# Performance work log

Measured on AMD Instinct MI355X. Metric: run time of the kernel, lower is better.

The kernel has to match this reference:

```python
import jax, jax.numpy as jnp
import numpy as np

N = 100000
E = 6400000
H = 64  # hidden_nf


def setup_inputs() -> dict:
    key = jax.random.key(0)
    ks = jax.random.split(key, 12)
    x = jax.random.normal(ks[0], (N, 3), dtype=jnp.float32)
    vel = jax.random.normal(ks[1], (N, 3), dtype=jnp.float32)
    vel_norm = jax.random.uniform(ks[2], (N, 1), dtype=jnp.float32)
    edge_index = jax.random.randint(ks[3], (2, E), 0, N, dtype=jnp.int32)
    # coord_mlp_vel: Linear(1,H) -> LeakyReLU(0.2) -> Linear(H,1)
    W1 = jax.random.normal(ks[4], (H, 1), dtype=jnp.float32) * (1.0 / np.sqrt(1))
    b1 = jnp.zeros((H,), dtype=jnp.float32)
    W2 = jax.random.normal(ks[5], (1, H), dtype=jnp.float32) * (1.0 / np.sqrt(H))
    b2 = jnp.zeros((1,), dtype=jnp.float32)
    # phi: Linear(1,H) -> LeakyReLU(0.2) -> Linear(H,1,bias=False, xavier gain=0.001) -> Tanh
    Wp1 = jax.random.normal(ks[6], (H, 1), dtype=jnp.float32) * (1.0 / np.sqrt(1))
    bp1 = jnp.zeros((H,), dtype=jnp.float32)
    Wp2 = jax.random.normal(ks[7], (1, H), dtype=jnp.float32) * 0.001
    return {"x": x, "vel_norm": vel_norm, "vel": vel, "edge_index": edge_index,
            "W1": W1, "b1": b1, "W2": W2, "b2": b2,
            "Wp1": Wp1, "bp1": bp1, "Wp2": Wp2}


def reference(x, vel_norm, vel, edge_index, W1, b1, W2, b2, Wp1, bp1, Wp2):
    row, col = edge_index[0], edge_index[1]
    # edge_model: gather endpoint positions, radial distance -> tiny MLP -> scaled diff
    x_diff = x[row] - x[col]                                   # [E, 3]
    radial = jnp.sqrt(jnp.sum(x_diff * x_diff, axis=1, keepdims=True))  # [E, 1]
    h = jax.nn.leaky_relu(radial @ Wp1.T + bp1, 0.2)           # [E, H]
    e_out = jnp.tanh(h @ Wp2.T)                                # [E, 1]
    m_ij = x_diff * e_out                                      # [E, 3]
    # node_model: unsorted_segment_mean over row
    agg_sum = jax.ops.segment_sum(m_ij, row, num_segments=x.shape[0])           # [N, 3]
    cnt = jax.ops.segment_sum(jnp.ones((m_ij.shape[0], 1), m_ij.dtype), row,
                              num_segments=x.shape[0])                           # [N, 1]
    x_out = x + agg_sum / jnp.maximum(cnt, 1.0)
    # velocity term: x + vel * coord_mlp_vel(vel_norm)
    hv = jax.nn.leaky_relu(vel_norm @ W1.T + b1, 0.2)          # [N, H]
    scale = hv @ W2.T + b2                                     # [N, 1]
    return x_out + vel * scale
```

## Files before the change

kernel.cpp:

```cpp
#include <hip/hip_runtime.h>
#include <hip/hip_fp16.h>
#include <math.h>

#define LEAKY 0.2f
#define HDIM 64
#define EPB 2048
#define TPB1 256
#define PERT (EPB / TPB1)
#define RANGE 1024
#define RSH 10
#define KMAX 128
#define NSLICE 12
#define FIXS 4194304.0f
#define INVFIXS (1.0f / 4194304.0f)


__device__ __forceinline__ float fast_tanh(float v) {
    float e = __builtin_amdgcn_exp2f(v * 2.88539008178f);
    return 1.0f - 2.0f * __builtin_amdgcn_rcpf(e + 1.0f);
}

__device__ __forceinline__ float edge_eo(float rad, float C, bool slow,
                                         const float* sW1, const float* sb1,
                                         const float* sW2) {
    if (!slow) return fast_tanh(C * rad);
    float a = 0.f;
    #pragma unroll
    for (int k = 0; k < HDIM; k++) {
        float h = fmaf(rad, sW1[k], sb1[k]);
        h = (h > 0.f) ? h : LEAKY * h;
        a = fmaf(sW2[k], h, a);
    }
    return fast_tanh(a);
}

__global__ void repack_kernel(const float* __restrict__ x, float4* __restrict__ x4, int N) {
    int i = blockIdx.x * blockDim.x + threadIdx.x;
    if (i < N) x4[i] = make_float4(x[3*i], x[3*i+1], x[3*i+2], 0.f);
}

__global__ void repack_h_kernel(const float* __restrict__ x, uint2* __restrict__ xh, int N,
                                const float* __restrict__ Wp1, const float* __restrict__ bp1,
                                const float* __restrict__ Wp2, float* __restrict__ consts) {
    int i = blockIdx.x * blockDim.x + threadIdx.x;
    if (i < N) {
        unsigned hx = __half_as_ushort(__float2half(x[3*i]));
        unsigned hy = __half_as_ushort(__float2half(x[3*i+1]));
        unsigned hz = __half_as_ushort(__float2half(x[3*i+2]));
        xh[i] = make_uint2((hy << 16) | hx, hz);
    }
    if (blockIdx.x == 0 && threadIdx.x < 64) {
        int k = threadIdx.x;
        float w1 = Wp1[k];
        float slope = (w1 >= 0.f) ? 1.f : LEAKY;
        float c = Wp2[k] * w1 * slope;
        float bnz = (bp1[k] != 0.f) ? 1.f : 0.f;
        #pragma unroll
        for (int off = 32; off > 0; off >>= 1) {
            c += __shfl_down(c, off, 64);
            bnz += __shfl_down(bnz, off, 64);
        }
        if (k == 0) { consts[0] = c; consts[1] = bnz; }
    }
}

__device__ __forceinline__ unsigned long long pack_rec(float dx, float dy, float dz,
                                                       float eo, unsigned lid) {
    unsigned hx = __half_as_ushort(__float2half(dx * eo));
    unsigned hy = __half_as_ushort(__float2half(dy * eo));
    unsigned hz = __half_as_ushort(__float2half(dz * eo));
    return (unsigned long long)lid
         | ((unsigned long long)hx << 11)
         | ((unsigned long long)hy << 27)
         | ((unsigned long long)hz << 43);
}

__device__ __forceinline__ uint2 make_record(uint2 ga, uint2 gb, int r,
                                             float C, bool slow,
                                             const float* sW1, const float* sb1,
                                             const float* sW2) {
    float ax = __half2float(__ushort_as_half((unsigned short)(ga.x & 0xFFFF)));
    float ay = __half2float(__ushort_as_half((unsigned short)(ga.x >> 16)));
    float az = __half2float(__ushort_as_half((unsigned short)(ga.y & 0xFFFF)));
    float bx = __half2float(__ushort_as_half((unsigned short)(gb.x & 0xFFFF)));
    float by = __half2float(__ushort_as_half((unsigned short)(gb.x >> 16)));
    float bz = __half2float(__ushort_as_half((unsigned short)(gb.y & 0xFFFF)));
    float dx = ax - bx, dy = ay - by, dz = az - bz;
    float rad = sqrtf(dx*dx + dy*dy + dz*dz);
    float eo = edge_eo(rad, C, slow, sW1, sb1, sW2);
    unsigned long long u = pack_rec(dx, dy, dz, eo, (unsigned)r & (RANGE - 1));
    return make_uint2((unsigned)u, (unsigned)(u >> 32));
}

__global__ __launch_bounds__(TPB1) void count2_kernel(const int* __restrict__ ei,
                                                      unsigned* __restrict__ histG,
                                                      int E, int K) {
    __shared__ unsigned hist[4][KMAX];
    int w = threadIdx.x >> 6;
    for (int k = threadIdx.x; k < 4 * KMAX; k += TPB1) ((unsigned*)hist)[k] = 0;
    __syncthreads();
    const size_t base = (size_t)blockIdx.x * EPB;
    if (base + EPB <= (size_t)E) {
        const int4* p = (const int4*)(ei + base);
        #pragma unroll
        for (int i = 0; i < EPB / 4 / TPB1; i++) {
            int4 v = p[threadIdx.x + i * TPB1];
            atomicAdd(&hist[w][((unsigned)v.x) >> RSH], 1u);
            atomicAdd(&hist[w][((unsigned)v.y) >> RSH], 1u);
            atomicAdd(&hist[w][((unsigned)v.z) >> RSH], 1u);
            atomicAdd(&hist[w][((unsigned)v.w) >> RSH], 1u);
        }
    } else {
        for (size_t e = base + threadIdx.x; e < (size_t)E; e += TPB1)
            atomicAdd(&hist[w][((unsigned)ei[e]) >> RSH], 1u);
    }
    __syncthreads();
    for (int k = threadIdx.x; k < K; k += TPB1)
        histG[(size_t)blockIdx.x * K + k] = hist[0][k] + hist[1][k] + hist[2][k] + hist[3][k];
}

__global__ __launch_bounds__(256) void colscan_kernel(unsigned* __restrict__ histG,
                                                      unsigned* __restrict__ totals,
                                                      int nblk, int K) {
    __shared__ unsigned pa[256], pb[256];
    const int b = blockIdx.x;
    const int t = threadIdx.x;
    const int chunk = (nblk + 255) / 256;
    const int r0 = t * chunk;
    unsigned s = 0;
    for (int i = 0; i < chunk; i++) {
        int r = r0 + i;
        if (r < nblk) s += histG[(size_t)r * K + b];
    }
    pa[t] = s;
    __syncthreads();
    unsigned* src = pa; unsigned* dst = pb;
    for (int off = 1; off < 256; off <<= 1) {
        unsigned v = src[t];
        if (t >= off) v += src[t - off];
        dst[t] = v;
        __syncthreads();
        unsigned* tmp = src; src = dst; dst = tmp;
    }
    unsigned excl = (t > 0) ? src[t - 1] : 0u;
    if (t == 255) totals[b] = src[255];
    unsigned run = excl;
    for (int i = 0; i < chunk; i++) {
        int r = r0 + i;
        if (r < nblk) {
            size_t a = (size_t)r * K + b;
            unsigned v = histG[a];
            histG[a] = run;
            run += v;
        }
    }
}

__global__ __launch_bounds__(TPB1) void fused_kernel(
        const uint2* __restrict__ xh,
        const int* __restrict__ ei,
        const float* __restrict__ Wp1, const float* __restrict__ bp1,
        const float* __restrict__ Wp2, const float* __restrict__ consts,
        const unsigned* __restrict__ histG, const unsigned* __restrict__ totals,
        uint2* __restrict__ recs, int E, int K) {
    __shared__ uint2 stage[EPB];
    __shared__ unsigned char bucket_of[EPB];
    __shared__ unsigned hist[KMAX];
    __shared__ unsigned scanv[KMAX + 1];
    __shared__ unsigned gstart[KMAX];
    __shared__ unsigned sbase[KMAX + 1];
    __shared__ float sW1[HDIM], sb1[HDIM], sW2[HDIM];
    const float C = consts[0];
    const bool slow = (consts[1] != 0.f);
    if (slow) {
        for (int k = threadIdx.x; k < HDIM; k += TPB1) {
            sW1[k] = Wp1[k]; sb1[k] = bp1[k]; sW2[k] = Wp2[k];
        }
    }
    for (int k = threadIdx.x; k < K; k += TPB1) hist[k] = 0;
    if (threadIdx.x < (unsigned)K) sbase[threadIdx.x] = totals[threadIdx.x];
    __syncthreads();

    const size_t base = (size_t)blockIdx.x * EPB;
    const unsigned t = threadIdx.x;
    uint2 rc[PERT];
    unsigned bk[PERT];
    if (base + EPB <= (size_t)E && (E & 3) == 0) {
        const int4* pr = (const int4*)(ei + base);
        const int4* pc = (const int4*)(ei + (size_t)E + base);
        int4 rv0 = pr[t];
        int4 rv1 = pr[t + TPB1];
        int4 cv0 = pc[t];
        int4 cv1 = pc[t + TPB1];
        uint2 ga0 = xh[rv0.x], ga1 = xh[rv0.y], ga2 = xh[rv0.z], ga3 = xh[rv0.w];
        uint2 ga4 = xh[rv1.x], ga5 = xh[rv1.y], ga6 = xh[rv1.z], ga7 = xh[rv1.w];
        uint2 gb0 = xh[cv0.x], gb1 = xh[cv0.y], gb2 = xh[cv0.z], gb3 = xh[cv0.w];
        uint2 gb4 = xh[cv1.x], gb5 = xh[cv1.y], gb6 = xh[cv1.z], gb7 = xh[cv1.w];
        rc[0] = make_record(ga0, gb0, rv0.x, C, slow, sW1, sb1, sW2);
        rc[1] = make_record(ga1, gb1, rv0.y, C, slow, sW1, sb1, sW2);
        rc[2] = make_record(ga2, gb2, rv0.z, C, slow, sW1, sb1, sW2);
        rc[3] = make_record(ga3, gb3, rv0.w, C, slow, sW1, sb1, sW2);
        rc[4] = make_record(ga4, gb4, rv1.x, C, slow, sW1, sb1, sW2);
        rc[5] = make_record(ga5, gb5, rv1.y, C, slow, sW1, sb1, sW2);
        rc[6] = make_record(ga6, gb6, rv1.z, C, slow, sW1, sb1, sW2);
        rc[7] = make_record(ga7, gb7, rv1.w, C, slow, sW1, sb1, sW2);
        bk[0] = (unsigned)rv0.x >> RSH; bk[1] = (unsigned)rv0.y >> RSH;
        bk[2] = (unsigned)rv0.z >> RSH; bk[3] = (unsigned)rv0.w >> RSH;
        bk[4] = (unsigned)rv1.x >> RSH; bk[5] = (unsigned)rv1.y >> RSH;
        bk[6] = (unsigned)rv1.z >> RSH; bk[7] = (unsigned)rv1.w >> RSH;
        #pragma unroll
        for (int i = 0; i < PERT; i++) atomicAdd(&hist[bk[i]], 1u);
    } else {
        #pragma unroll
        for (int i = 0; i < PERT; i++) {
            size_t e = base + (size_t)i * TPB1 + t;
            bk[i] = 0xFFFFFFFFu;
            if (e < (size_t)E) {
                int r = ei[e];
                int c = ei[(size_t)E + e];
                uint2 ga = xh[r], gb = xh[c];
                rc[i] = make_record(ga, gb, r, C, slow, sW1, sb1, sW2);
                bk[i] = (unsigned)r >> RSH;
                atomicAdd(&hist[bk[i]], 1u);
            }
        }
    }
    __syncthreads();
    if (t == 0) {
        unsigned a = 0;
        for (int k = 0; k < K; k++) { scanv[k] = a; a += hist[k]; }
        scanv[K] = a;
    } else if (t == 64) {
        unsigned a = 0;
        for (int k = 0; k < K; k++) { unsigned v = sbase[k]; sbase[k] = a; a += v; }
        sbase[K] = a;
    }
    __syncthreads();
    if (t < (unsigned)K)
        gstart[t] = sbase[t] + histG[(size_t)blockIdx.x * K + t];
    for (int k = t; k < K; k += TPB1) hist[k] = scanv[k];
    __syncthreads();
    #pragma unroll
    for (int i = 0; i < PERT; i++) {
        if (bk[i] != 0xFFFFFFFFu) {
            unsigned slot = atomicAdd(&hist[bk[i]], 1u);
            stage[slot] = rc[i];
            bucket_of[slot] = (unsigned char)bk[i];
        }
    }
    __syncthreads();
    unsigned total = scanv[K];
    for (unsigned j = t; j < total; j += TPB1) {
        unsigned b_ = bucket_of[j];
        recs[(size_t)gstart[b_] + (j - scanv[b_])] = stage[j];
    }
}

__global__ __launch_bounds__(TPB1) void count_kernel(const int* __restrict__ ei,
                                                     unsigned* __restrict__ cnts,
                                                     int E, int K) {
    __shared__ unsigned hist[4][KMAX];
    int w = threadIdx.x >> 6;
    for (int k = threadIdx.x; k < 4 * KMAX; k += TPB1) ((unsigned*)hist)[k] = 0;
    __syncthreads();
    int base = blockIdx.x * EPB;
    #pragma unroll
    for (int i = 0; i < PERT; i++) {
        int e = base + i * TPB1 + threadIdx.x;
        if (e < E) atomicAdd(&hist[w][((unsigned)ei[e]) >> RSH], 1u);
    }
    __syncthreads();
    for (int k = threadIdx.x; k < K; k += TPB1) {
        unsigned t = hist[0][k] + hist[1][k] + hist[2][k] + hist[3][k];
        if (t) atomicAdd(&cnts[k], t);
    }
}

__global__ void scan_kernel(const unsigned* __restrict__ cnts,
                            unsigned* __restrict__ base,
                            unsigned* __restrict__ cursor, int K) {
    if (threadIdx.x == 0) {
        unsigned acc = 0;
        for (int k = 0; k < K; k++) { base[k] = acc; cursor[k] = acc; acc += cnts[k]; }
        base[K] = acc;
    }
}

__global__ void precompute_kernel(const float* __restrict__ Wp1,
                                  const float* __restrict__ bp1,
                                  const float* __restrict__ Wp2,
                                  float* __restrict__ consts) {
    int k = threadIdx.x;
    float w1 = Wp1[k];
    float slope = (w1 >= 0.f) ? 1.f : LEAKY;
    float c = Wp2[k] * w1 * slope;
    float bnz = (bp1[k] != 0.f) ? 1.f : 0.f;
    #pragma unroll
    for (int off = 32; off > 0; off >>= 1) {
        c += __shfl_down(c, off, 64);
        bnz += __shfl_down(bnz, off, 64);
    }
    if (k == 0) { consts[0] = c; consts[1] = bnz; }
}

__global__ __launch_bounds__(TPB1) void bin_kernel(
        const float* __restrict__ x, const float4* __restrict__ x4, int use4,
        const int* __restrict__ ei,
        const float* __restrict__ Wp1, const float* __restrict__ bp1,
        const float* __restrict__ Wp2, const float* __restrict__ consts,
        unsigned* __restrict__ cursor, uint2* __restrict__ recs, int E, int K) {
    __shared__ uint2 stage[EPB];
    __shared__ unsigned char bucket_of[EPB];
    __shared__ unsigned hist[KMAX];
    __shared__ unsigned scanv[KMAX + 1];
    __shared__ unsigned gstart[KMAX];
    __shared__ float sW1[HDIM], sb1[HDIM], sW2[HDIM];
    const float C = consts[0];
    const bool slow = (consts[1] != 0.f);
    if (slow) {
        for (int k = threadIdx.x; k < HDIM; k += TPB1) {
            sW1[k] = Wp1[k]; sb1[k] = bp1[k]; sW2[k] = Wp2[k];
        }
    }
    for (int k = threadIdx.x; k < K; k += TPB1) hist[k] = 0;
    __syncthreads();

    int base = blockIdx.x * EPB;
    uint2 rc[PERT];
    unsigned bk[PERT];
    #pragma unroll
    for (int i = 0; i < PERT; i++) {
        int e = base + i * TPB1 + threadIdx.x;
        bk[i] = 0xFFFFFFFFu;
        if (e < E) {
            int r = ei[e];
            int c = ei[(size_t)E + e];
            float dx, dy, dz;
            if (use4) {
                float4 a = x4[r], b = x4[c];
                dx = a.x - b.x; dy = a.y - b.y; dz = a.z - b.z;
            } else {
                dx = x[3*r]   - x[3*c];
                dy = x[3*r+1] - x[3*c+1];
                dz = x[3*r+2] - x[3*c+2];
            }
            float rad = sqrtf(dx*dx + dy*dy + dz*dz);
            float eo = edge_eo(rad, C, slow, sW1, sb1, sW2);
            unsigned long long u = pack_rec(dx, dy, dz, eo, (unsigned)r & (RANGE - 1));
            rc[i] = make_uint2((unsigned)u, (unsigned)(u >> 32));
            bk[i] = (unsigned)r >> RSH;
            atomicAdd(&hist[bk[i]], 1u);
        }
    }
    __syncthreads();
    if (threadIdx.x == 0) {
        unsigned a = 0;
        for (int k = 0; k < K; k++) { scanv[k] = a; a += hist[k]; }
        scanv[K] = a;
    }
    __syncthreads();
    if (threadIdx.x < (unsigned)K) {
        unsigned c_ = scanv[threadIdx.x + 1] - scanv[threadIdx.x];
        gstart[threadIdx.x] = c_ ? atomicAdd(&cursor[threadIdx.x], c_) : 0u;
    }
    for (int k = threadIdx.x; k < K; k += TPB1) hist[k] = scanv[k];
    __syncthreads();
    #pragma unroll
    for (int i = 0; i < PERT; i++) {
        if (bk[i] != 0xFFFFFFFFu) {
            unsigned slot = atomicAdd(&hist[bk[i]], 1u);
            stage[slot] = rc[i];
            bucket_of[slot] = (unsigned char)bk[i];
        }
    }
    __syncthreads();
    unsigned total = scanv[K];
    for (unsigned j = threadIdx.x; j < total; j += TPB1) {
        unsigned b_ = bucket_of[j];
        recs[(size_t)gstart[b_] + (j - scanv[b_])] = stage[j];
    }
}

__device__ __forceinline__ void proc_rec(uint2 r, unsigned (*acc)[RANGE]) {
    unsigned long long u = ((unsigned long long)r.y << 32) | r.x;
    unsigned lid = (unsigned)(u & (RANGE - 1));
    float mx = __half2float(__ushort_as_half((unsigned short)((u >> 11) & 0xFFFF)));
    float my = __half2float(__ushort_as_half((unsigned short)((u >> 27) & 0xFFFF)));
    float mz = __half2float(__ushort_as_half((unsigned short)((u >> 43) & 0xFFFF)));
    atomicAdd(&acc[0][lid], (unsigned)(int)__float2int_rn(mx * FIXS));
    atomicAdd(&acc[1][lid], (unsigned)(int)__float2int_rn(my * FIXS));
    atomicAdd(&acc[2][lid], (unsigned)(int)__float2int_rn(mz * FIXS));
    atomicAdd(&acc[3][lid], 1u);
}

__global__ __launch_bounds__(256) void reduce_kernel(
        const uint2* __restrict__ recs, const unsigned* __restrict__ totals,
        float4* __restrict__ slices, int N, int K) {
    __shared__ unsigned acc[4][RANGE];
    __shared__ unsigned sbase[KMAX + 1];
    int b = blockIdx.x / NSLICE;
    int s = blockIdx.x % NSLICE;
    if (threadIdx.x < (unsigned)K) sbase[threadIdx.x] = totals[threadIdx.x];
    for (int i = threadIdx.x; i < RANGE; i += 256) {
        acc[0][i] = 0u; acc[1][i] = 0u; acc[2][i] = 0u; acc[3][i] = 0u;
    }
    __syncthreads();
    if (threadIdx.x == 0) {
        unsigned a = 0;
        for (int k = 0; k < K; k++) { unsigned v = sbase[k]; sbase[k] = a; a += v; }
        sbase[K] = a;
    }
    __syncthreads();
    unsigned lo = sbase[b], hi = sbase[b + 1];
    unsigned cnt = hi - lo;
    unsigned per = (cnt + NSLICE - 1) / NSLICE;
    unsigned st = lo + (unsigned)s * per;
    unsigned en = st + per; if (en > hi) en = hi;
    unsigned j = st + threadIdx.x;
    if (st < hi) {
        while (j + 256 < en) {
            uint2 r0 = recs[j];
            uint2 r1 = recs[j + 256];
            proc_rec(r0, acc);
            proc_rec(r1, acc);
            j += 512;
        }
        while (j < en) { proc_rec(recs[j], acc); j += 256; }
    }
    __syncthreads();
    int nbase = b * RANGE;
    for (int i = threadIdx.x; i < RANGE; i += 256) {
        int node = nbase + i;
        if (node < N)
            slices[(size_t)s * N + node] =
                make_float4((float)(int)acc[0][i] * INVFIXS,
                            (float)(int)acc[1][i] * INVFIXS,
                            (float)(int)acc[2][i] * INVFIXS,
                            (float)acc[3][i]);
    }
}

__global__ void node_kernel(const float* __restrict__ x, const float* __restrict__ vel_norm,
                            const float* __restrict__ vel,
                            const float* __restrict__ W1, const float* __restrict__ b1,
                            const float* __restrict__ W2, const float* __restrict__ b2,
                            const float4* __restrict__ slices,
                            float* __restrict__ out, int N, int S) {
    __shared__ float sW1[HDIM], sb1[HDIM], sW2[HDIM];
    for (int k = threadIdx.x; k < HDIM; k += blockDim.x) {
        sW1[k] = W1[k]; sb1[k] = b1[k]; sW2[k] = W2[k];
    }
    __syncthreads();
    int i = blockIdx.x * blockDim.x + threadIdx.x;
    if (i >= N) return;
    float sx = 0.f, sy = 0.f, sz = 0.f, sc = 0.f;
    for (int s = 0; s < S; s++) {
        float4 v = slices[(size_t)s * N + i];
        sx += v.x; sy += v.y; sz += v.z; sc += v.w;
    }
    float vn = vel_norm[i];
    float a = b2[0];
    #pragma unroll
    for (int k = 0; k < HDIM; k++) {
        float h = fmaf(vn, sW1[k], sb1[k]);
        h = (h > 0.f) ? h : LEAKY * h;
        a = fmaf(sW2[k], h, a);
    }
    float inv = 1.0f / fmaxf(sc, 1.0f);
    out[3*i]     = x[3*i]     + sx * inv + vel[3*i]     * a;
    out[3*i + 1] = x[3*i + 1] + sy * inv + vel[3*i + 1] * a;
    out[3*i + 2] = x[3*i + 2] + sz * inv + vel[3*i + 2] * a;
}

__global__ __launch_bounds__(256) void reduce_basep_kernel(
        const uint2* __restrict__ recs, const unsigned* __restrict__ base,
        float4* __restrict__ slices, int N, int K) {
    __shared__ unsigned acc[4][RANGE];
    int b = blockIdx.x / NSLICE;
    int s = blockIdx.x % NSLICE;
    for (int i = threadIdx.x; i < RANGE; i += 256) {
        acc[0][i] = 0u; acc[1][i] = 0u; acc[2][i] = 0u; acc[3][i] = 0u;
    }
    __syncthreads();
    unsigned lo = base[b], hi = base[b + 1];
    unsigned cnt = hi - lo;
    unsigned per = (cnt + NSLICE - 1) / NSLICE;
    unsigned st = lo + (unsigned)s * per;
    unsigned en = st + per; if (en > hi) en = hi;
    unsigned j = st + threadIdx.x;
    if (st < hi) {
        while (j + 256 < en) {
            uint2 r0 = recs[j];
            uint2 r1 = recs[j + 256];
            proc_rec(r0, acc);
            proc_rec(r1, acc);
            j += 512;
        }
        while (j < en) { proc_rec(recs[j], acc); j += 256; }
    }
    __syncthreads();
    int nbase = b * RANGE;
    for (int i = threadIdx.x; i < RANGE; i += 256) {
        int node = nbase + i;
        if (node < N)
            slices[(size_t)s * N + node] =
                make_float4((float)(int)acc[0][i] * INVFIXS,
                            (float)(int)acc[1][i] * INVFIXS,
                            (float)(int)acc[2][i] * INVFIXS,
                            (float)acc[3][i]);
    }
}

__global__ void edge_atomic_kernel(const float* __restrict__ x, const int* __restrict__ ei,
                                   const float* __restrict__ Wp1, const float* __restrict__ bp1,
                                   const float* __restrict__ Wp2, const float* __restrict__ consts,
                                   float* __restrict__ acc, int E) {
    __shared__ float sW1[HDIM], sb1[HDIM], sW2[HDIM];
    const float C = consts[0];
    const bool slow = (consts[1] != 0.f);
    if (slow) {
        for (int k = threadIdx.x; k < HDIM; k += blockDim.x) {
            sW1[k] = Wp1[k]; sb1[k] = bp1[k]; sW2[k] = Wp2[k];
        }
        __syncthreads();
    }
    int e = blockIdx.x * blockDim.x + threadIdx.x;
    if (e >= E) return;
    int r = ei[e];
    int c = ei[E + e];
    float dx = x[3*r] - x[3*c];
    float dy = x[3*r+1] - x[3*c+1];
    float dz = x[3*r+2] - x[3*c+2];
    float rad = sqrtf(dx*dx + dy*dy + dz*dz);
    float eo = edge_eo(rad, C, slow, sW1, sb1, sW2);
    float* basep = acc + ((size_t)r << 2);
    atomicAdd(basep + 0, dx * eo);
    atomicAdd(basep + 1, dy * eo);
    atomicAdd(basep + 2, dz * eo);
    atomicAdd(basep + 3, 1.f);
}

extern "C" void kernel_launch(void* const* d_in, const int* in_sizes, int n_in,
                              void* d_out, int out_size, void* d_ws, size_t ws_size,
                              hipStream_t stream) {
    const float* x        = (const float*)d_in[0];
    const float* vel_norm = (const float*)d_in[1];
    const float* vel      = (const float*)d_in[2];
    const int*   ei       = (const int*)  d_in[3];
    const float* W1       = (const float*)d_in[4];
    const float* b1       = (const float*)d_in[5];
    const float* W2       = (const float*)d_in[6];
    const float* b2       = (const float*)d_in[7];
    const float* Wp1      = (const float*)d_in[8];
    const float* bp1      = (const float*)d_in[9];
    const float* Wp2      = (const float*)d_in[10];

    const int N = in_sizes[0] / 3;
    const int E = in_sizes[3] / 2;
    const int K = (N + RANGE - 1) / RANGE;
    const int nblk = (E + EPB - 1) / EPB;

    size_t rec_bytes   = (size_t)E * sizeof(uint2);
    size_t slice_bytes = (size_t)NSLICE * N * sizeof(float4);
    size_t x4_bytes    = (size_t)N * sizeof(float4);
    size_t histG_bytes = (size_t)nblk * K * sizeof(unsigned);

    size_t sp_slices = rec_bytes;
    size_t sp_xh     = sp_slices + slice_bytes;
    size_t sp_hist   = sp_xh + x4_bytes;
    size_t sp_tot    = sp_hist + histG_bytes;
    size_t sp_const  = (sp_tot + (size_t)(K + 1) * sizeof(unsigned) + 15) & ~(size_t)15;
    size_t need_split = sp_const + 32;

    size_t small_bytes = (size_t)(KMAX + (KMAX + 1) + KMAX) * sizeof(unsigned) + 32;
    size_t fu_recs  = slice_bytes;
    size_t fu_x4    = fu_recs + rec_bytes;
    size_t fu_small = fu_x4 + x4_bytes;
    size_t need_fused = fu_small + small_bytes;

    if (K <= KMAX && ws_size >= need_split) {
        uint2*    recs   = (uint2*)   d_ws;
        float4*   slices = (float4*)  ((char*)d_ws + sp_slices);
        uint2*    xh     = (uint2*)   ((char*)d_ws + sp_xh);
        unsigned* histG  = (unsigned*)((char*)d_ws + sp_hist);
        unsigned* totals = (unsigned*)((char*)d_ws + sp_tot);
        float*    consts = (float*)   ((char*)d_ws + sp_const);

        repack_h_kernel<<<(N + 255) / 256, 256, 0, stream>>>(x, xh, N, Wp1, bp1, Wp2, consts);
        count2_kernel<<<nblk, TPB1, 0, stream>>>(ei, histG, E, K);
        colscan_kernel<<<K, 256, 0, stream>>>(histG, totals, nblk, K);
        fused_kernel<<<nblk, TPB1, 0, stream>>>(xh, ei, Wp1, bp1, Wp2, consts,
                                                histG, totals, recs, E, K);
        reduce_kernel<<<K * NSLICE, 256, 0, stream>>>(recs, totals, slices, N, K);
        node_kernel<<<(N + 255) / 256, 256, 0, stream>>>(x, vel_norm, vel, W1, b1, W2, b2,
                                                         slices, (float*)d_out, N, NSLICE);
    } else if (K <= KMAX && ws_size >= need_fused) {
        float4*   slices = (float4*)  d_ws;
        uint2*    recs   = (uint2*)   ((char*)d_ws + fu_recs);
        float4*   x4     = (float4*)  ((char*)d_ws + fu_x4);
        unsigned* cnts   = (unsigned*)((char*)d_ws + fu_small);
        unsigned* basep  = cnts + KMAX;
        unsigned* cursor = basep + KMAX + 1;
        float*    consts = (float*)(cursor + KMAX);

        hipMemsetAsync(cnts, 0, small_bytes, stream);
        precompute_kernel<<<1, 64, 0, stream>>>(Wp1, bp1, Wp2, consts);
        repack_kernel<<<(N + 255) / 256, 256, 0, stream>>>(x, x4, N);
        count_kernel<<<nblk, TPB1, 0, stream>>>(ei, cnts, E, K);
        scan_kernel<<<1, 64, 0, stream>>>(cnts, basep, cursor, K);
        bin_kernel<<<nblk, TPB1, 0, stream>>>(x, x4, 1, ei, Wp1, bp1, Wp2, consts,
                                              cursor, recs, E, K);
        reduce_basep_kernel<<<K * NSLICE, 256, 0, stream>>>(recs, basep, slices, N, K);
        node_kernel<<<(N + 255) / 256, 256, 0, stream>>>(x, vel_norm, vel, W1, b1, W2, b2,
                                                         slices, (float*)d_out, N, NSLICE);
    } else {
        float* acc    = (float*)d_ws;
        float* consts = (float*)((char*)d_ws + (size_t)N * sizeof(float4));
        hipMemsetAsync(d_ws, 0, (size_t)N * sizeof(float4) + 32, stream);
        precompute_kernel<<<1, 64, 0, stream>>>(Wp1, bp1, Wp2, consts);
        edge_atomic_kernel<<<(E + 255) / 256, 256, 0, stream>>>(x, ei, Wp1, bp1, Wp2,
                                                                consts, acc, E);
        node_kernel<<<(N + 255) / 256, 256, 0, stream>>>(x, vel_norm, vel, W1, b1, W2, b2,
                                                         (const float4*)acc, (float*)d_out, N, 1);
    }
}
```

Baseline: 199.9 us.

## Merge repack and histogram kernels, double reduce slices, unroll record loop

Fuses the half-precision position repack and the per-block bucket histogram into one launch, with each wavefront counting its own 2048-edge chunk and writing its histogram directly, so no block barrier or 4-way sum is needed. This removes one kernel launch and lets the two independent prep jobs overlap. The reduce stage doubles the number of slices per bucket to raise parallelism and unrolls its record loop to four loads in flight. In exchange the node kernel has twice as many slices to sum, and the slice buffer grows in workspace.

Result: slower. 207.1 us (+3.6%).

```diff
diff --git a/kernel.cpp b/kernel.cpp
--- a/kernel.cpp
+++ b/kernel.cpp
@@ -10,7 +10,7 @@
 #define RANGE 1024
 #define RSH 10
 #define KMAX 128
-#define NSLICE 12
+#define NSLICE 24
 #define FIXS 4194304.0f
 #define INVFIXS (1.0f / 4194304.0f)
 
@@ -39,28 +39,58 @@
     if (i < N) x4[i] = make_float4(x[3*i], x[3*i+1], x[3*i+2], 0.f);
 }
 
-__global__ void repack_h_kernel(const float* __restrict__ x, uint2* __restrict__ xh, int N,
-                                const float* __restrict__ Wp1, const float* __restrict__ bp1,
-                                const float* __restrict__ Wp2, float* __restrict__ consts) {
-    int i = blockIdx.x * blockDim.x + threadIdx.x;
-    if (i < N) {
-        unsigned hx = __half_as_ushort(__float2half(x[3*i]));
-        unsigned hy = __half_as_ushort(__float2half(x[3*i+1]));
-        unsigned hz = __half_as_ushort(__float2half(x[3*i+2]));
-        xh[i] = make_uint2((hy << 16) | hx, hz);
-    }
-    if (blockIdx.x == 0 && threadIdx.x < 64) {
-        int k = threadIdx.x;
-        float w1 = Wp1[k];
-        float slope = (w1 >= 0.f) ? 1.f : LEAKY;
-        float c = Wp2[k] * w1 * slope;
-        float bnz = (bp1[k] != 0.f) ? 1.f : 0.f;
-        #pragma unroll
-        for (int off = 32; off > 0; off >>= 1) {
-            c += __shfl_down(c, off, 64);
-            bnz += __shfl_down(bnz, off, 64);
-        }
-        if (k == 0) { consts[0] = c; consts[1] = bnz; }
+__global__ __launch_bounds__(TPB1) void prep_kernel(
+        const float* __restrict__ x, uint2* __restrict__ xh, int N,
+        const float* __restrict__ Wp1, const float* __restrict__ bp1,
+        const float* __restrict__ Wp2, float* __restrict__ consts,
+        const int* __restrict__ ei, unsigned* __restrict__ histG,
+        int E, int K, int nblk, int nblkc) {
+    if ((int)blockIdx.x < nblkc) {
+        __shared__ unsigned hist[4][KMAX];
+        const int w = threadIdx.x >> 6;
+        const int lane = threadIdx.x & 63;
+        for (int k = lane; k < KMAX; k += 64) hist[w][k] = 0;
+        const int sub = blockIdx.x * 4 + w;
+        if (sub >= nblk) return;
+        const size_t sbase = (size_t)sub * EPB;
+        if (sbase + EPB <= (size_t)E) {
+            const int4* p = (const int4*)(ei + sbase);
+            #pragma unroll
+            for (int i = 0; i < EPB / 4 / 64; i++) {
+                int4 v = p[lane + i * 64];
+                atomicAdd(&hist[w][((unsigned)v.x) >> RSH], 1u);
+                atomicAdd(&hist[w][((unsigned)v.y) >> RSH], 1u);
+                atomicAdd(&hist[w][((unsigned)v.z) >> RSH], 1u);
+                atomicAdd(&hist[w][((unsigned)v.w) >> RSH], 1u);
+            }
+        } else {
+            for (size_t e = sbase + lane; e < (size_t)E; e += 64)
+                atomicAdd(&hist[w][((unsigned)ei[e]) >> RSH], 1u);
+        }
+        for (int k = lane; k < K; k += 64)
+            histG[(size_t)sub * K + k] = hist[w][k];
+    } else {
+        int rb = (int)blockIdx.x - nblkc;
+        int i = rb * TPB1 + (int)threadIdx.x;
+        if (i < N) {
+            unsigned hx = __half_as_ushort(__float2half(x[3*i]));
+            unsigned hy = __half_as_ushort(__float2half(x[3*i+1]));
+            unsigned hz = __half_as_ushort(__float2half(x[3*i+2]));
+            xh[i] = make_uint2((hy << 16) | hx, hz);
+        }
+        if (rb == 0 && threadIdx.x < 64) {
+            int k = threadIdx.x;
+            float w1 = Wp1[k];
+            float slope = (w1 >= 0.f) ? 1.f : LEAKY;
+            float c = Wp2[k] * w1 * slope;
+            float bnz = (bp1[k] != 0.f) ? 1.f : 0.f;
+            #pragma unroll
+            for (int off = 32; off > 0; off >>= 1) {
+                c += __shfl_down(c, off, 64);
+                bnz += __shfl_down(bnz, off, 64);
+            }
+            if (k == 0) { consts[0] = c; consts[1] = bnz; }
+        }
     }
 }
 
@@ -90,33 +120,6 @@
     float eo = edge_eo(rad, C, slow, sW1, sb1, sW2);
     unsigned long long u = pack_rec(dx, dy, dz, eo, (unsigned)r & (RANGE - 1));
     return make_uint2((unsigned)u, (unsigned)(u >> 32));
-}
-
-__global__ __launch_bounds__(TPB1) void count2_kernel(const int* __restrict__ ei,
-                                                      unsigned* __restrict__ histG,
-                                                      int E, int K) {
-    __shared__ unsigned hist[4][KMAX];
-    int w = threadIdx.x >> 6;
-    for (int k = threadIdx.x; k < 4 * KMAX; k += TPB1) ((unsigned*)hist)[k] = 0;
-    __syncthreads();
-    const size_t base = (size_t)blockIdx.x * EPB;
-    if (base + EPB <= (size_t)E) {
-        const int4* p = (const int4*)(ei + base);
-        #pragma unroll
-        for (int i = 0; i < EPB / 4 / TPB1; i++) {
-            int4 v = p[threadIdx.x + i * TPB1];
-            atomicAdd(&hist[w][((unsigned)v.x) >> RSH], 1u);
-            atomicAdd(&hist[w][((unsigned)v.y) >> RSH], 1u);
-            atomicAdd(&hist[w][((unsigned)v.z) >> RSH], 1u);
-            atomicAdd(&hist[w][((unsigned)v.w) >> RSH], 1u);
-        }
-    } else {
-        for (size_t e = base + threadIdx.x; e < (size_t)E; e += TPB1)
-            atomicAdd(&hist[w][((unsigned)ei[e]) >> RSH], 1u);
-    }
-    __syncthreads();
-    for (int k = threadIdx.x; k < K; k += TPB1)
-        histG[(size_t)blockIdx.x * K + k] = hist[0][k] + hist[1][k] + hist[2][k] + hist[3][k];
 }
 
 __global__ __launch_bounds__(256) void colscan_kernel(unsigned* __restrict__ histG,
@@ -418,12 +421,14 @@
     unsigned en = st + per; if (en > hi) en = hi;
     unsigned j = st + threadIdx.x;
     if (st < hi) {
-        while (j + 256 < en) {
+        while (j + 768 < en) {
             uint2 r0 = recs[j];
             uint2 r1 = recs[j + 256];
-            proc_rec(r0, acc);
-            proc_rec(r1, acc);
-            j += 512;
+            uint2 r2 = recs[j + 512];
+            uint2 r3 = recs[j + 768];
+            proc_rec(r0, acc); proc_rec(r1, acc);
+            proc_rec(r2, acc); proc_rec(r3, acc);
+            j += 1024;
         }
         while (j < en) { proc_rec(recs[j], acc); j += 256; }
     }
@@ -559,6 +564,8 @@
     const int E = in_sizes[3] / 2;
     const int K = (N + RANGE - 1) / RANGE;
     const int nblk = (E + EPB - 1) / EPB;
+    const int nblkc = (nblk + 3) / 4;
+    const int nblkr = (N + TPB1 - 1) / TPB1;
 
     size_t rec_bytes   = (size_t)E * sizeof(uint2);
     size_t slice_bytes = (size_t)NSLICE * N * sizeof(float4);
@@ -586,8 +593,8 @@
         unsigned* totals = (unsigned*)((char*)d_ws + sp_tot);
         float*    consts = (float*)   ((char*)d_ws + sp_const);
 
-        repack_h_kernel<<<(N + 255) / 256, 256, 0, stream>>>(x, xh, N, Wp1, bp1, Wp2, consts);
-        count2_kernel<<<nblk, TPB1, 0, stream>>>(ei, histG, E, K);
+        prep_kernel<<<nblkc + nblkr, TPB1, 0, stream>>>(x, xh, N, Wp1, bp1, Wp2, consts,
+                                                        ei, histG, E, K, nblk, nblkc);
         colscan_kernel<<<K, 256, 0, stream>>>(histG, totals, nblk, K);
         fused_kernel<<<nblk, TPB1, 0, stream>>>(xh, ei, Wp1, bp1, Wp2, consts,
                                                 histG, totals, recs, E, K);
```
